# Kernel optimization log

Hardware: AMD Instinct MI355X
Metric: run time of the kernel (lower is better)

## Reference

```python
import jax, jax.numpy as jnp
import numpy as np

SOS_TOKEN = 1


def setup_inputs() -> dict:
    key = jax.random.key(0)
    L, B, H, V = 2, 32, 512, 32000
    ks = jax.random.split(key, 8)
    s = 1.0 / np.sqrt(H)
    return {
        "encoder_hidden": jax.random.normal(ks[0], (L, B, H), jnp.float32),
        "embedding": jax.random.normal(ks[1], (V, H), jnp.float32) * s,
        "W_ih": jax.random.normal(ks[2], (L, 4 * H, H), jnp.float32) * s,
        "W_hh": jax.random.normal(ks[3], (L, 4 * H, H), jnp.float32) * s,
        "b_ih": jax.random.normal(ks[4], (L, 4 * H), jnp.float32) * s,
        "b_hh": jax.random.normal(ks[5], (L, 4 * H), jnp.float32) * s,
        "W_out": jax.random.normal(ks[6], (V, H), jnp.float32) * s,
        "b_out": jax.random.normal(ks[7], (V,), jnp.float32) * s,
        "target_length": 128,
    }


def _lstm_cell(x, h, c, W_ih_l, W_hh_l, b_ih_l, b_hh_l):
    # PyTorch gate order: i, f, g, o
    gates = x @ W_ih_l.T + b_ih_l + h @ W_hh_l.T + b_hh_l  # [B, 4H]
    i, f, g, o = jnp.split(gates, 4, axis=-1)
    c_new = jax.nn.sigmoid(f) * c + jax.nn.sigmoid(i) * jnp.tanh(g)
    h_new = jax.nn.sigmoid(o) * jnp.tanh(c_new)
    return h_new, c_new


def reference(encoder_hidden, embedding, W_ih, W_hh, b_ih, b_hh, W_out, b_out, target_length):
    L, B, H = encoder_hidden.shape
    h0 = encoder_hidden                      # [L, B, H]
    c0 = jnp.zeros_like(encoder_hidden)      # wrapper passes zeros for c0
    tok0 = jnp.full((B,), SOS_TOKEN, dtype=jnp.int32)

    def step(carry, _):
        tok, h, c = carry
        x = jax.nn.relu(embedding[tok])      # [B, H] embed + ReLU
        hs, cs = [], []
        inp = x
        for l in range(L):                   # small fixed layer loop
            h_l, c_l = _lstm_cell(inp, h[l], c[l], W_ih[l], W_hh[l], b_ih[l], b_hh[l])
            hs.append(h_l)
            cs.append(c_l)
            inp = h_l
        logits = inp @ W_out.T + b_out       # [B, V]
        logp = jax.nn.log_softmax(logits, axis=-1)
        next_tok = jnp.argmax(logp, axis=-1).astype(jnp.int32)  # greedy top-1 (detach)
        return (next_tok, jnp.stack(hs), jnp.stack(cs)), logp

    (_, hT, cT), logps = jax.lax.scan(step, (tok0, h0, c0), None, length=target_length)
    outputs = jnp.transpose(logps, (1, 0, 2))  # [B, T, V] (cat along dim=1)
    return outputs, hT, cT
```

## Files before the change

kernel.cpp:

```cpp
#include <hip/hip_runtime.h>
#include <math.h>

#define Gz   250
#define NTz  512
#define Bz   32
#define Hz   512
#define Vz   32000
#define Tz   128
#define VBz  128
#define BHz  (Bz*Hz)
#define LBHz (2*BHz)
#define BTVz ((size_t)Bz*(size_t)Tz*(size_t)Vz)

#define WS_BAR  0
#define WS_ASUM 2048
#define WS_AMAX 10240
#define WS_H    26624

#define L_HSA    0
#define L_HSB    65536
#define L_LOGITS 131072
#define L_SPART  131072
#define L_PMAX   147584
#define L_PSUM   151680
#define L_REDM   153728
#define L_REDS   155776
#define L_BIAS   156800
#define L_LOGZ   156864
#define L_TOK    156992
#define L_C      157120
#define L_TOTAL  158144

typedef unsigned long long ull;
typedef float f32x4 __attribute__((ext_vector_type(4)));

__device__ __forceinline__ float sigmf(float x) { return 1.0f / (1.0f + expf(-x)); }

__device__ __forceinline__ ull bp8(const float* p) {
  return __hip_atomic_load((const ull*)p, __ATOMIC_RELAXED, __HIP_MEMORY_SCOPE_AGENT);
}
__device__ __forceinline__ void cstore(float* p, float v) {
  __hip_atomic_store(p, v, __ATOMIC_RELAXED, __HIP_MEMORY_SCOPE_AGENT);
}
__device__ __forceinline__ ull packlm(float x, int v) {
  unsigned u = __float_as_uint(x);
  u = (u & 0x80000000u) ? ~u : (u | 0x80000000u);
  return ((ull)u << 32) | (unsigned)(Vz - 1 - v);
}
__device__ __forceinline__ int hoff(int b, int k) { return (b << 9) + (k ^ ((b & 15) << 2)); }

__device__ __forceinline__ void grid_barrier(unsigned* bar, int bid) {
  __syncthreads();
  if (threadIdx.x == 0) {
    unsigned* gen = bar + 257;
    unsigned g = __hip_atomic_load(gen, __ATOMIC_RELAXED, __HIP_MEMORY_SCOPE_AGENT);
    const int gi = bid & 7;
    const unsigned gsz = (unsigned)(Gz >> 3) + (((unsigned)gi < (Gz & 7u)) ? 1u : 0u);
    unsigned prev = __hip_atomic_fetch_add(&bar[gi * 32], 1u, __ATOMIC_RELAXED, __HIP_MEMORY_SCOPE_AGENT);
    if (prev == gsz - 1u) {
      __hip_atomic_store(&bar[gi * 32], 0u, __ATOMIC_RELAXED, __HIP_MEMORY_SCOPE_AGENT);
      asm volatile("s_waitcnt vmcnt(0)" ::: "memory");
      unsigned pm = __hip_atomic_fetch_add(&bar[256], 1u, __ATOMIC_RELAXED, __HIP_MEMORY_SCOPE_AGENT);
      if (pm == 7u) {
        __hip_atomic_store(&bar[256], 0u, __ATOMIC_RELAXED, __HIP_MEMORY_SCOPE_AGENT);
        asm volatile("s_waitcnt vmcnt(0)" ::: "memory");
        __hip_atomic_store(gen, g + 1u, __ATOMIC_RELAXED, __HIP_MEMORY_SCOPE_AGENT);
      }
    }
    while (__hip_atomic_load(gen, __ATOMIC_RELAXED, __HIP_MEMORY_SCOPE_AGENT) == g)
      __builtin_amdgcn_s_sleep(1);
  }
  __syncthreads();
}

__device__ __forceinline__ void stage_rows(const float* __restrict__ src, float* lds, int tid) {
  #pragma unroll
  for (int it = 0; it < 16; ++it) {
    int f = (it * NTz + tid) << 1;
    int b = f >> 9, k = f & 511;
    ull v = bp8(src + f);
    *(ull*)(lds + hoff(b, k)) = v;
  }
}

template<bool X_FROM_EMB>
__device__ __forceinline__ void lstm_phase(
    int tid, int hblk,
    const float* __restrict__ emb, const int* s_tok_,
    const float* xlds, const float* hlds,
    const float* __restrict__ Wih, const float* __restrict__ Whh,
    const float* __restrict__ bih, const float* __restrict__ bhh,
    float* s_part_, float* s_bias_, float* c_l,
    float* hdst)
{
  if (tid < 16) {
    int gate = tid >> 2, hl = tid & 3;
    int j = gate * Hz + (hblk << 2) + hl;
    s_bias_[tid] = bih[j] + bhh[j];
  }
  const int b = tid & 31, kq = (tid >> 5) & 7, rp = tid >> 8;
  const int k0 = kq * 64;
  const int swz = (b & 15) << 2;

  const float* wiA = Wih + (size_t)(2 * rp * Hz + (hblk << 2)) * Hz + k0;
  const float* whA = Whh + (size_t)(2 * rp * Hz + (hblk << 2)) * Hz + k0;

  const float* xbase; const float* hbase = hlds + (b << 9);
  if (X_FROM_EMB) xbase = emb + (size_t)s_tok_[b] * Hz + k0;
  else            xbase = xlds + (b << 9);

  float acc[8];
  #pragma unroll
  for (int r = 0; r < 8; ++r) acc[r] = 0.f;

  #pragma unroll 2
  for (int c = 0; c < 64; c += 4) {
    float x0, x1, x2, x3;
    if (X_FROM_EMB) {
      float4 xv = *(const float4*)(xbase + c);
      x0 = fmaxf(xv.x, 0.f); x1 = fmaxf(xv.y, 0.f);
      x2 = fmaxf(xv.z, 0.f); x3 = fmaxf(xv.w, 0.f);
    } else {
      float4 xv = *(const float4*)(xbase + ((k0 + c) ^ swz));
      x0 = xv.x; x1 = xv.y; x2 = xv.z; x3 = xv.w;
    }
    float4 hv = *(const float4*)(hbase + ((k0 + c) ^ swz));
    #pragma unroll
    for (int r = 0; r < 8; ++r) {
      const size_t off = (size_t)(r >> 2) * (Hz * Hz) + (size_t)(r & 3) * Hz + c;
      float4 wiv = *(const float4*)(wiA + off);
      float4 whv = *(const float4*)(whA + off);
      acc[r] += x0 * wiv.x + x1 * wiv.y + x2 * wiv.z + x3 * wiv.w
              + hv.x * whv.x + hv.y * whv.y + hv.z * whv.z + hv.w * whv.w;
    }
  }
  #pragma unroll
  for (int r = 0; r < 8; ++r)
    s_part_[((rp * 8 + r) * 32 + b) * 8 + kq] = acc[r];
  __syncthreads();
  {
    int row = tid >> 5, bb = tid & 31;
    float s = s_bias_[row];
    #pragma unroll
    for (int q = 0; q < 8; ++q) s += s_part_[(row * 32 + bb) * 8 + q];
    s_part_[(row * 32 + bb) * 8] = s;
  }
  __syncthreads();
  if (tid < 128) {
    int hl = tid >> 5, bb = tid & 31;
    float gi = s_part_[((0 * 4 + hl) * 32 + bb) * 8];
    float gf = s_part_[((1 * 4 + hl) * 32 + bb) * 8];
    float gg = s_part_[((2 * 4 + hl) * 32 + bb) * 8];
    float go = s_part_[((3 * 4 + hl) * 32 + bb) * 8];
    float c_old = c_l[hl * 32 + bb];
    float cn = sigmf(gf) * c_old + sigmf(gi) * tanhf(gg);
    c_l[hl * 32 + bb] = cn;
    cstore(hdst + bb * Hz + (hblk << 2) + hl, sigmf(go) * tanhf(cn));
  }
}

__device__ __forceinline__ void tok_reduce(int tid, float* acc_sum, ull* acc_max,
                                           float* redS, ull* redM, float* logZ, int* tok) {
  if (tid < 256) {
    int b = tid & 31, g = tid >> 5;
    float s = 0.f; ull m = 0ull;
    #pragma unroll
    for (int u = 0; u < 8; ++u) {
      int bk = g * 8 + u;
      s += __hip_atomic_load(&acc_sum[bk * Bz + b], __ATOMIC_RELAXED, __HIP_MEMORY_SCOPE_AGENT);
      ull x = __hip_atomic_load(&acc_max[bk * Bz + b], __ATOMIC_RELAXED, __HIP_MEMORY_SCOPE_AGENT);
      m = x > m ? x : m;
    }
    redS[g * Bz + b] = s; redM[g * Bz + b] = m;
  }
  __syncthreads();
  if (tid < 32) {
    float s = 0.f; ull m = 0ull;
    #pragma unroll
    for (int g = 0; g < 8; ++g) {
      s += redS[g * Bz + tid];
      ull x = redM[g * Bz + tid]; m = x > m ? x : m;
    }
    logZ[tid] = logf(s);
    tok[tid] = (Vz - 1) - (int)(unsigned)(m & 0xFFFFFFFFull);
  }
  __syncthreads();
}

__device__ __forceinline__ void write_logp(int tid, int v0, int tstep,
                                           const float* logits_, const float* logZ_, float* out) {
  #pragma unroll
  for (int i = 0; i < 2; ++i) {
    int pos = ((i * NTz) + tid) * 4;
    int b = pos >> 7, v = pos & 127;
    float lz = logZ_[b];
    f32x4 rr;
    rr.x = logits_[b * 129 + v]     - lz;
    rr.y = logits_[b * 129 + v + 1] - lz;
    rr.z = logits_[b * 129 + v + 2] - lz;
    rr.w = logits_[b * 129 + v + 3] - lz;
    __builtin_nontemporal_store(rr,
        (f32x4*)(out + (size_t)b * ((size_t)Tz * Vz) + (size_t)tstep * Vz + v0 + v));
  }
}

__global__ void rnn_init(const float* __restrict__ enc, float* __restrict__ ws) {
  int i = blockIdx.x * blockDim.x + threadIdx.x;
  float* hs = (float*)((char*)ws + WS_H);
  if (i < LBHz) hs[i] = enc[i];
  if (i < 2048) {
    ((float*)((char*)ws + WS_ASUM))[i] = 0.f;
    ((ull*)((char*)ws + WS_AMAX))[i] = 0ull;
  }
  if (i < 512) ((unsigned*)ws)[i] = 0u;
}

#define WL(r, J) (*(const f32x4*)(wr##r + (((J + kq) & 7) << 2)))
#define P3J(J) { \
  const int kk = (kq << 5) + (((J + kq) & 7) << 2); \
  f32x4 h4 = *(const f32x4*)(hb + (kk ^ swz)); \
  a0 += h4 * w0##J; a1 += h4 * w1##J; a2 += h4 * w2##J; a3 += h4 * w3##J; }

__global__ __launch_bounds__(NTz)
__attribute__((amdgpu_waves_per_eu(2, 2)))
void rnn_decode(
    const float* __restrict__ emb,  const float* __restrict__ Wih,
    const float* __restrict__ Whh,  const float* __restrict__ bih,
    const float* __restrict__ bhh,  const float* __restrict__ Wout,
    const float* __restrict__ bout, float* __restrict__ out,
    float* __restrict__ ws)
{
  extern __shared__ char smem[];
  const int tid = threadIdx.x;
  const int bid = blockIdx.x;

  unsigned* bar  = (unsigned*)ws;
  float* acc_sum = (float*)((char*)ws + WS_ASUM);
  ull*   acc_max = (ull*)((char*)ws + WS_AMAX);
  float* hbufs   = (float*)((char*)ws + WS_H);

  float* hsA    = (float*)(smem + L_HSA);
  float* hsB    = (float*)(smem + L_HSB);
  float* logits = (float*)(smem + L_LOGITS);
  float* s_part = (float*)(smem + L_SPART);
  ull*   pmax   = (ull*)(smem + L_PMAX);
  float* psum   = (float*)(smem + L_PSUM);
  ull*   redM   = (ull*)(smem + L_REDM);
  float* redS   = (float*)(smem + L_REDS);
  float* s_bias = (float*)(smem + L_BIAS);
  float* s_logZ = (float*)(smem + L_LOGZ);
  int*   s_tok  = (int*)(smem + L_TOK);
  float* s_c    = (float*)(smem + L_C);

  const int v0 = bid * VBz;
  if (tid < 256) s_c[tid] = 0.f;
  __syncthreads();

  const int vg = tid >> 4, kq = tid & 15;
  f32x4 w00, w01, w02, w03, w04, w05, w06, w07;
  f32x4 w10, w11, w12, w13, w14, w15, w16, w17;
  f32x4 w20, w21, w22, w23, w24, w25, w26, w27;
  f32x4 w30, w31, w32, w33, w34, w35, w36, w37;
  {
    const float* wr0 = Wout + (size_t)(v0 + (vg << 2) + 0) * Hz + (kq << 5);
    const float* wr1 = Wout + (size_t)(v0 + (vg << 2) + 1) * Hz + (kq << 5);
    const float* wr2 = Wout + (size_t)(v0 + (vg << 2) + 2) * Hz + (kq << 5);
    const float* wr3 = Wout + (size_t)(v0 + (vg << 2) + 3) * Hz + (kq << 5);
    w00 = WL(0,0); w01 = WL(0,1); w02 = WL(0,2); w03 = WL(0,3);
    w04 = WL(0,4); w05 = WL(0,5); w06 = WL(0,6); w07 = WL(0,7);
    w10 = WL(1,0); w11 = WL(1,1); w12 = WL(1,2); w13 = WL(1,3);
    w14 = WL(1,4); w15 = WL(1,5); w16 = WL(1,6); w17 = WL(1,7);
    w20 = WL(2,0); w21 = WL(2,1); w22 = WL(2,2); w23 = WL(2,3);
    w24 = WL(2,4); w25 = WL(2,5); w26 = WL(2,6); w27 = WL(2,7);
    w30 = WL(3,0); w31 = WL(3,1); w32 = WL(3,2); w33 = WL(3,3);
    w34 = WL(3,4); w35 = WL(3,5); w36 = WL(3,6); w37 = WL(3,7);
  }

  for (int t = 0; t < Tz; ++t) {
    asm volatile("" : "+v"(w00),"+v"(w01),"+v"(w02),"+v"(w03),
                      "+v"(w04),"+v"(w05),"+v"(w06),"+v"(w07));
    asm volatile("" : "+v"(w10),"+v"(w11),"+v"(w12),"+v"(w13),
                      "+v"(w14),"+v"(w15),"+v"(w16),"+v"(w17));
    asm volatile("" : "+v"(w20),"+v"(w21),"+v"(w22),"+v"(w23),
                      "+v"(w24),"+v"(w25),"+v"(w26),"+v"(w27));
    asm volatile("" : "+v"(w30),"+v"(w31),"+v"(w32),"+v"(w33),
                      "+v"(w34),"+v"(w35),"+v"(w36),"+v"(w37));

    float* h_old = hbufs + (t & 1) * LBHz;
    float* h_new = hbufs + ((t + 1) & 1) * LBHz;

    if (bid < 128) stage_rows(h_old, hsA, tid);
    if (t == 0) {
      if (tid < 32) s_tok[tid] = 1;
    } else {
      tok_reduce(tid, acc_sum, acc_max, redS, redM, s_logZ, s_tok);
      write_logp(tid, v0, t - 1, logits, s_logZ, out);
    }
    __syncthreads();
    if (bid < 128)
      lstm_phase<true>(tid, bid, emb, s_tok, nullptr, hsA,
                       Wih, Whh, bih, bhh, s_part, s_bias, s_c, h_new);
    grid_barrier(bar, bid);

    if (bid < 128) {
      stage_rows(h_new, hsB, tid);
      stage_rows(h_old + BHz, hsA, tid);
      __syncthreads();
      lstm_phase<false>(tid, bid, nullptr, nullptr, hsB, hsA,
                        Wih + (size_t)2048 * Hz, Whh + (size_t)2048 * Hz,
                        bih + 2048, bhh + 2048, s_part, s_bias, s_c + 128, h_new + BHz);
    } else if (bid == 128) {
      for (int u = tid; u < 2048; u += NTz) {
        __hip_atomic_store(&acc_sum[u], 0.f, __ATOMIC_RELAXED, __HIP_MEMORY_SCOPE_AGENT);
        __hip_atomic_store(&acc_max[u], 0ull, __ATOMIC_RELAXED, __HIP_MEMORY_SCOPE_AGENT);
      }
    }
    grid_barrier(bar, bid);

    stage_rows(h_new + BHz, hsA, tid);
    __syncthreads();
    {
      const float b_r0 = bout[v0 + (vg << 2)];
      const float b_r1 = bout[v0 + (vg << 2) + 1];
      const float b_r2 = bout[v0 + (vg << 2) + 2];
      const float b_r3 = bout[v0 + (vg << 2) + 3];
      #pragma unroll 2
      for (int b = 0; b < 32; ++b) {
        const float* hb = hsA + (b << 9);
        const int swz = (b & 15) << 2;
        f32x4 a0 = (f32x4)0.f, a1 = (f32x4)0.f, a2 = (f32x4)0.f, a3 = (f32x4)0.f;
        P3J(0) P3J(1) P3J(2) P3J(3) P3J(4) P3J(5) P3J(6) P3J(7)
        float s0 = (a0.x + a0.y) + (a0.z + a0.w);
        float s1 = (a1.x + a1.y) + (a1.z + a1.w);
        float s2 = (a2.x + a2.y) + (a2.z + a2.w);
        float s3 = (a3.x + a3.y) + (a3.z + a3.w);
        #pragma unroll
        for (int m = 1; m < 16; m <<= 1) {
          s0 += __shfl_xor(s0, m);
          s1 += __shfl_xor(s1, m);
          s2 += __shfl_xor(s2, m);
          s3 += __shfl_xor(s3, m);
        }
        if (kq == 0) {
          logits[b * 129 + (vg << 2)]     = s0 + b_r0;
          logits[b * 129 + (vg << 2) + 1] = s1 + b_r1;
          logits[b * 129 + (vg << 2) + 2] = s2 + b_r2;
          logits[b * 129 + (vg << 2) + 3] = s3 + b_r3;
        }
      }
    }
    __syncthreads();
    {
      const int b2 = tid & 31, ch = tid >> 5;
      float m = -3.0e38f; int argv = 0; float s = 0.f;
      #pragma unroll
      for (int u = 0; u < 8; ++u) {
        int vl = ch * 8 + u;
        float x = logits[b2 * 129 + vl];
        s += expf(x);
        if (x > m) { m = x; argv = vl; }
      }
      pmax[ch * 32 + b2] = packlm(m, v0 + argv);
      psum[ch * 32 + b2] = s;
    }
    __syncthreads();
    if (tid < 32) {
      ull m = 0ull; float s = 0.f;
      #pragma unroll
      for (int ch = 0; ch < 16; ++ch) {
        ull x = pmax[ch * 32 + tid]; m = x > m ? x : m;
        s += psum[ch * 32 + tid];
      }
      atomicAdd(&acc_sum[(bid & 63) * Bz + tid], s);
      atomicMax(&acc_max[(bid & 63) * Bz + tid], m);
    }
    grid_barrier(bar, bid);
  }

  tok_reduce(tid, acc_sum, acc_max, redS, redM, s_logZ, s_tok);
  write_logp(tid, v0, Tz - 1, logits, s_logZ, out);
  if (bid >= 128 && bid < 144) {
    int f = (bid - 128) * 2048 + tid * 4;
    ull a = bp8(hbufs + f), b = bp8(hbufs + f + 2);
    *(ull*)(out + BTVz + f) = a;
    *(ull*)(out + BTVz + f + 2) = b;
  }
  if (bid < 128 && tid < 256) {
    int l = tid >> 7, hl = (tid >> 5) & 3, bb = tid & 31;
    out[BTVz + LBHz + (size_t)l * BHz + (size_t)bb * Hz + (bid << 2) + hl] =
        s_c[l * 128 + hl * 32 + bb];
  }
}

extern "C" void kernel_launch(void* const* d_in, const int* in_sizes, int n_in,
                              void* d_out, int out_size, void* d_ws, size_t ws_size,
                              hipStream_t stream) {
  (void)in_sizes; (void)n_in; (void)out_size; (void)ws_size;
  const float* enc  = (const float*)d_in[0];
  const float* emb  = (const float*)d_in[1];
  const float* Wih  = (const float*)d_in[2];
  const float* Whh  = (const float*)d_in[3];
  const float* bih  = (const float*)d_in[4];
  const float* bhh  = (const float*)d_in[5];
  const float* Wout = (const float*)d_in[6];
  const float* bout = (const float*)d_in[7];
  float* out = (float*)d_out;
  float* ws  = (float*)d_ws;

  (void)hipFuncSetAttribute((const void*)rnn_decode,
                            hipFuncAttributeMaxDynamicSharedMemorySize, L_TOTAL);
  rnn_init<<<64, 512, 0, stream>>>(enc, ws);
  rnn_decode<<<Gz, NTz, L_TOTAL, stream>>>(emb, Wih, Whh, bih, bhh, Wout, bout, out, ws);
}
```

Measured before the change: 14.11 ms.

## Cut per-step global staging and shrink softmax accumulator slots to 16

The layer-1 hidden buffers now stay resident in LDS across steps, so each step stages two hidden-state matrices instead of four. Staging uses 16-byte loads with the sc1 cache-bypass bit in inline asm instead of 8-byte atomic loads. The cross-block sum/max accumulators drop from 64 slots to 16, so the token reduction becomes a single vectorised load pass with fewer zeroing stores. In exchange, more blocks contend on each atomic slot, and correctness now depends on the LDS buffer roles being swapped consistently.

```diff
diff --git a/kernel.cpp b/kernel.cpp
--- a/kernel.cpp
+++ b/kernel.cpp
@@ -14,8 +14,8 @@
 
 #define WS_BAR  0
 #define WS_ASUM 2048
-#define WS_AMAX 10240
-#define WS_H    26624
+#define WS_AMAX 4096
+#define WS_H    8192
 
 #define L_HSA    0
 #define L_HSB    65536
@@ -23,8 +23,6 @@
 #define L_SPART  131072
 #define L_PMAX   147584
 #define L_PSUM   151680
-#define L_REDM   153728
-#define L_REDS   155776
 #define L_BIAS   156800
 #define L_LOGZ   156864
 #define L_TOK    156992
@@ -33,6 +31,7 @@
 
 typedef unsigned long long ull;
 typedef float f32x4 __attribute__((ext_vector_type(4)));
+typedef unsigned long long ull2 __attribute__((ext_vector_type(2)));
 
 __device__ __forceinline__ float sigmf(float x) { return 1.0f / (1.0f + expf(-x)); }
 
@@ -73,14 +72,36 @@
   __syncthreads();
 }
 
-__device__ __forceinline__ void stage_rows(const float* __restrict__ src, float* lds, int tid) {
-  #pragma unroll
-  for (int it = 0; it < 16; ++it) {
-    int f = (it * NTz + tid) << 1;
-    int b = f >> 9, k = f & 511;
-    ull v = bp8(src + f);
-    *(ull*)(lds + hoff(b, k)) = v;
-  }
+__device__ __forceinline__ void stage16(const float* __restrict__ src, float* lds, int tid) {
+  const float* q0 = src + ((0 * NTz + tid) << 2);
+  const float* q1 = src + ((1 * NTz + tid) << 2);
+  const float* q2 = src + ((2 * NTz + tid) << 2);
+  const float* q3 = src + ((3 * NTz + tid) << 2);
+  const float* q4 = src + ((4 * NTz + tid) << 2);
+  const float* q5 = src + ((5 * NTz + tid) << 2);
+  const float* q6 = src + ((6 * NTz + tid) << 2);
+  const float* q7 = src + ((7 * NTz + tid) << 2);
+  f32x4 a0, a1, a2, a3, b0, b1, b2, b3;
+  asm volatile(
+      "global_load_dwordx4 %0, %4, off sc1\n\t"
+      "global_load_dwordx4 %1, %5, off sc1\n\t"
+      "global_load_dwordx4 %2, %6, off sc1\n\t"
+      "global_load_dwordx4 %3, %7, off sc1"
+      : "=&v"(a0), "=&v"(a1), "=&v"(a2), "=&v"(a3)
+      : "v"(q0), "v"(q1), "v"(q2), "v"(q3) : "memory");
+  asm volatile(
+      "global_load_dwordx4 %0, %4, off sc1\n\t"
+      "global_load_dwordx4 %1, %5, off sc1\n\t"
+      "global_load_dwordx4 %2, %6, off sc1\n\t"
+      "global_load_dwordx4 %3, %7, off sc1\n\t"
+      "s_waitcnt vmcnt(0)"
+      : "=&v"(b0), "=&v"(b1), "=&v"(b2), "=&v"(b3)
+      : "v"(q4), "v"(q5), "v"(q6), "v"(q7) : "memory");
+  #define ST16(IT, R) { int f = ((IT * NTz + tid) << 2); \
+    *(f32x4*)(lds + hoff(f >> 9, f & 511)) = R; }
+  ST16(0, a0) ST16(1, a1) ST16(2, a2) ST16(3, a3)
+  ST16(4, b0) ST16(5, b1) ST16(6, b2) ST16(7, b3)
+  #undef ST16
 }
 
 template<bool X_FROM_EMB>
@@ -159,27 +180,31 @@
   }
 }
 
-__device__ __forceinline__ void tok_reduce(int tid, float* acc_sum, ull* acc_max,
-                                           float* redS, ull* redM, float* logZ, int* tok) {
-  if (tid < 256) {
-    int b = tid & 31, g = tid >> 5;
-    float s = 0.f; ull m = 0ull;
-    #pragma unroll
-    for (int u = 0; u < 8; ++u) {
-      int bk = g * 8 + u;
-      s += __hip_atomic_load(&acc_sum[bk * Bz + b], __ATOMIC_RELAXED, __HIP_MEMORY_SCOPE_AGENT);
-      ull x = __hip_atomic_load(&acc_max[bk * Bz + b], __ATOMIC_RELAXED, __HIP_MEMORY_SCOPE_AGENT);
-      m = x > m ? x : m;
-    }
-    redS[g * Bz + b] = s; redM[g * Bz + b] = m;
+__device__ __forceinline__ void tok_reduce2(int tid, const float* acc_sum, const ull* acc_max,
+                                            float* redS, ull* redM, float* logZ, int* tok) {
+  if (tid < 128) {
+    int g = tid >> 3, b4 = (tid & 7) << 2;
+    const float* p = acc_sum + (g << 5) + b4;
+    f32x4 v;
+    asm volatile("global_load_dwordx4 %0, %1, off sc1\n\ts_waitcnt vmcnt(0)"
+                 : "=&v"(v) : "v"(p) : "memory");
+    *(f32x4*)(redS + (g << 5) + b4) = v;
+  } else if (tid < 384) {
+    int u = tid - 128;
+    int g = u >> 4, b2 = (u & 15) << 1;
+    const ull* p = acc_max + (g << 5) + b2;
+    ull2 m;
+    asm volatile("global_load_dwordx4 %0, %1, off sc1\n\ts_waitcnt vmcnt(0)"
+                 : "=&v"(m) : "v"(p) : "memory");
+    *(ull2*)(redM + (g << 5) + b2) = m;
   }
   __syncthreads();
   if (tid < 32) {
     float s = 0.f; ull m = 0ull;
     #pragma unroll
-    for (int g = 0; g < 8; ++g) {
-      s += redS[g * Bz + tid];
-      ull x = redM[g * Bz + tid]; m = x > m ? x : m;
+    for (int g = 0; g < 16; ++g) {
+      s += redS[(g << 5) + tid];
+      ull x = redM[(g << 5) + tid]; m = x > m ? x : m;
     }
     logZ[tid] = logf(s);
     tok[tid] = (Vz - 1) - (int)(unsigned)(m & 0xFFFFFFFFull);
@@ -208,10 +233,7 @@
   int i = blockIdx.x * blockDim.x + threadIdx.x;
   float* hs = (float*)((char*)ws + WS_H);
   if (i < LBHz) hs[i] = enc[i];
-  if (i < 2048) {
-    ((float*)((char*)ws + WS_ASUM))[i] = 0.f;
-    ((ull*)((char*)ws + WS_AMAX))[i] = 0ull;
-  }
+  if (i < 768) ((ull*)((char*)ws + WS_ASUM))[i] = 0ull;
   if (i < 512) ((unsigned*)ws)[i] = 0u;
 }
 
@@ -245,8 +267,6 @@
   float* s_part = (float*)(smem + L_SPART);
   ull*   pmax   = (ull*)(smem + L_PMAX);
   float* psum   = (float*)(smem + L_PSUM);
-  ull*   redM   = (ull*)(smem + L_REDM);
-  float* redS   = (float*)(smem + L_REDS);
   float* s_bias = (float*)(smem + L_BIAS);
   float* s_logZ = (float*)(smem + L_LOGZ);
   int*   s_tok  = (int*)(smem + L_TOK);
@@ -276,6 +296,12 @@
     w34 = WL(3,4); w35 = WL(3,5); w36 = WL(3,6); w37 = WL(3,7);
   }
 
+  if (bid < 128) {
+    stage16(hbufs, hsA, tid);
+    stage16(hbufs + BHz, hsB, tid);
+  }
+  __syncthreads();
+
   for (int t = 0; t < Tz; ++t) {
     asm volatile("" : "+v"(w00),"+v"(w01),"+v"(w02),"+v"(w03),
                       "+v"(w04),"+v"(w05),"+v"(w06),"+v"(w07));
@@ -289,35 +315,33 @@
     float* h_old = hbufs + (t & 1) * LBHz;
     float* h_new = hbufs + ((t + 1) & 1) * LBHz;
 
-    if (bid < 128) stage_rows(h_old, hsA, tid);
     if (t == 0) {
       if (tid < 32) s_tok[tid] = 1;
+      __syncthreads();
     } else {
-      tok_reduce(tid, acc_sum, acc_max, redS, redM, s_logZ, s_tok);
+      tok_reduce2(tid, acc_sum, acc_max, psum, pmax, s_logZ, s_tok);
       write_logp(tid, v0, t - 1, logits, s_logZ, out);
-    }
-    __syncthreads();
+      __syncthreads();
+    }
     if (bid < 128)
       lstm_phase<true>(tid, bid, emb, s_tok, nullptr, hsA,
                        Wih, Whh, bih, bhh, s_part, s_bias, s_c, h_new);
     grid_barrier(bar, bid);
 
     if (bid < 128) {
-      stage_rows(h_new, hsB, tid);
-      stage_rows(h_old + BHz, hsA, tid);
+      stage16(h_new, hsA, tid);
       __syncthreads();
-      lstm_phase<false>(tid, bid, nullptr, nullptr, hsB, hsA,
+      lstm_phase<false>(tid, bid, nullptr, nullptr, hsA, hsB,
                         Wih + (size_t)2048 * Hz, Whh + (size_t)2048 * Hz,
                         bih + 2048, bhh + 2048, s_part, s_bias, s_c + 128, h_new + BHz);
     } else if (bid == 128) {
-      for (int u = tid; u < 2048; u += NTz) {
-        __hip_atomic_store(&acc_sum[u], 0.f, __ATOMIC_RELAXED, __HIP_MEMORY_SCOPE_AGENT);
-        __hip_atomic_store(&acc_max[u], 0ull, __ATOMIC_RELAXED, __HIP_MEMORY_SCOPE_AGENT);
-      }
+      ull* zb = (ull*)acc_sum;
+      for (int u = tid; u < 768; u += NTz)
+        __hip_atomic_store(&zb[u], 0ull, __ATOMIC_RELAXED, __HIP_MEMORY_SCOPE_AGENT);
     }
     grid_barrier(bar, bid);
 
-    stage_rows(h_new + BHz, hsA, tid);
+    stage16(h_new + BHz, hsB, tid);
     __syncthreads();
     {
       const float b_r0 = bout[v0 + (vg << 2)];
@@ -326,7 +350,7 @@
       const float b_r3 = bout[v0 + (vg << 2) + 3];
       #pragma unroll 2
       for (int b = 0; b < 32; ++b) {
-        const float* hb = hsA + (b << 9);
+        const float* hb = hsB + (b << 9);
         const int swz = (b & 15) << 2;
         f32x4 a0 = (f32x4)0.f, a1 = (f32x4)0.f, a2 = (f32x4)0.f, a3 = (f32x4)0.f;
         P3J(0) P3J(1) P3J(2) P3J(3) P3J(4) P3J(5) P3J(6) P3J(7)
@@ -371,13 +395,13 @@
         ull x = pmax[ch * 32 + tid]; m = x > m ? x : m;
         s += psum[ch * 32 + tid];
       }
-      atomicAdd(&acc_sum[(bid & 63) * Bz + tid], s);
-      atomicMax(&acc_max[(bid & 63) * Bz + tid], m);
+      atomicAdd(&acc_sum[((bid & 15) << 5) + tid], s);
+      atomicMax(&acc_max[((bid & 15) << 5) + tid], m);
     }
     grid_barrier(bar, bid);
   }
 
-  tok_reduce(tid, acc_sum, acc_max, redS, redM, s_logZ, s_tok);
+  tok_reduce2(tid, acc_sum, acc_max, psum, pmax, s_logZ, s_tok);
   write_logp(tid, v0, Tz - 1, logits, s_logZ, out);
   if (bid >= 128 && bid < 144) {
     int f = (bid - 128) * 2048 + tid * 4;
```

Result: faster. 12.01 ms (-14.9%).
